# Kernel optimization log

Measured on AMD Instinct MI355X. Metric: run time of the kernel, lower is better.

Reference implementation:

```python
import jax, jax.numpy as jnp
import numpy as np

L = 768
Z_DIM = 128
C = 32
EPS = 1e-5


def _layer_norm(x, w, b):
    mu = jnp.mean(x, axis=-1, keepdims=True)
    var = jnp.mean(jnp.square(x - mu), axis=-1, keepdims=True)
    return (x - mu) * jax.lax.rsqrt(var + EPS) * w + b


def setup_inputs() -> dict:
    key = jax.random.key(0)
    ks = jax.random.split(key, 12)
    s_z = 1.0 / np.sqrt(Z_DIM)
    s_c = 1.0 / np.sqrt(C)
    return {
        "z": jax.random.normal(ks[0], (L, L, Z_DIM), dtype=jnp.float32),
        "norm_w": jnp.ones((Z_DIM,), jnp.float32),
        "norm_b": jnp.zeros((Z_DIM,), jnp.float32),
        "onorm_w": jnp.ones((C,), jnp.float32),
        "onorm_b": jnp.zeros((C,), jnp.float32),
        "a_w": jax.random.normal(ks[1], (C, Z_DIM), jnp.float32) * s_z,
        "a_b": jnp.zeros((C,), jnp.float32),
        "ag_w": jax.random.normal(ks[2], (C, Z_DIM), jnp.float32) * s_z,
        "ag_b": jnp.zeros((C,), jnp.float32),
        "g_w": jax.random.normal(ks[3], (Z_DIM, Z_DIM), jnp.float32) * s_z,
        "g_b": jnp.zeros((Z_DIM,), jnp.float32),
        "o_w": jax.random.normal(ks[4], (Z_DIM, C), jnp.float32) * s_c,
        "o_b": jnp.zeros((Z_DIM,), jnp.float32),
    }


def reference(z, norm_w, norm_b, onorm_w, onorm_b, a_w, a_b, ag_w, ag_b, g_w, g_b, o_w, o_b):
    zn = _layer_norm(z, norm_w, norm_b)                       # [L,L,Z]
    a = (zn @ a_w.T + a_b) * jax.nn.sigmoid(zn @ ag_w.T + ag_b)  # [L,L,C]
    # source computes b with the same (a) projections -> b == a
    o = jnp.einsum('ilc,jlc->ijc', a, a)                      # [L,L,C]
    o = _layer_norm(o, onorm_w, onorm_b)
    o = o @ o_w.T + o_b                                        # [L,L,Z]
    o = o * jax.nn.sigmoid(zn @ g_w.T + g_b)
    return o
```

## Files before the change

kernel.cpp:

```cpp
#include <hip/hip_runtime.h>
#include <math.h>


#define LDIM 768
#define LL   (768 * 768)
#define ZD   128
#define CD   32

typedef __bf16 bf16x8 __attribute__((ext_vector_type(8)));
typedef float  f32x4  __attribute__((ext_vector_type(4)));

__device__ __forceinline__ ushort f2bf(float f) {
    __bf16 h = (__bf16)f;
    return __builtin_bit_cast(ushort, h);
}
__device__ __forceinline__ float bf2f(ushort u) {
    return __builtin_bit_cast(float, ((unsigned)u) << 16);
}
__device__ __forceinline__ float sigm(float x) {
    return __builtin_amdgcn_rcpf(1.0f + __expf(-x));
}

__global__ __launch_bounds__(256) void k0_wfrag(
    const float* __restrict__ aw, const float* __restrict__ agw,
    const float* __restrict__ gw, ushort* __restrict__ wfrag)
{
    const int f = blockIdx.x * 256 + threadIdx.x;
    if (f >= 12 * 4 * 64) return;
    const int n4 = f >> 6, lane = f & 63;
    const int n = n4 >> 2, kk = n4 & 3;
    const int fr = lane & 15, hi = lane >> 4;
    const int ch = n * 16 + fr;
    const int k0 = kk * 32 + hi * 8;
    const float* src = (ch < 32) ? (aw + ch * ZD)
                     : (ch < 64) ? (agw + (ch - 32) * ZD)
                                 : (gw + (ch - 64) * ZD);
    union { ushort us[8]; uint4 q; } pk;
    #pragma unroll
    for (int j = 0; j < 8; ++j) pk.us[j] = f2bf(src[k0 + j]);
    *(uint4*)&wfrag[(size_t)f * 8] = pk.q;
}

__global__ __launch_bounds__(256) void k1_ln_proj(
    const float* __restrict__ z, const float* __restrict__ nw, const float* __restrict__ nb,
    const ushort* __restrict__ wfrag,
    const float* __restrict__ ab, const float* __restrict__ agb, const float* __restrict__ gb,
    ushort* __restrict__ a_t, ushort* __restrict__ gate)
{
    __shared__ ushort zn[64][136];
    __shared__ ushort gl[64][136];

    const int tid = threadIdx.x;
    const int lane = tid & 63, wave = tid >> 6;
    const int fr = lane & 15, hi = lane >> 4;

    const int t0 = (wave < 2) ? wave     : 6 + (wave - 2) * 3;
    const int t1 = (wave < 2) ? wave + 2 : t0 + 1;
    const int t2 = (wave < 2) ? wave + 4 : t0 + 2;

    bf16x8 bv0[4], bv1[4], bv2[4];
    {
        const ushort* wl = wfrag + (size_t)lane * 8;
        #pragma unroll
        for (int kk = 0; kk < 4; ++kk) {
            bv0[kk] = *(const bf16x8*)(wl + (size_t)(t0 * 4 + kk) * 512);
            bv1[kk] = *(const bf16x8*)(wl + (size_t)(t1 * 4 + kk) * 512);
            bv2[kk] = *(const bf16x8*)(wl + (size_t)(t2 * 4 + kk) * 512);
        }
    }

    float abv = 0.f, agbv = 0.f, gbv0 = 0.f, gbv1 = 0.f, gbv2;
    if (wave < 2) {
        abv  = ab[wave * 16 + fr];
        agbv = agb[wave * 16 + fr];
        gbv2 = gb[t2 * 16 - 64 + fr];
    } else {
        gbv0 = gb[t0 * 16 - 64 + fr];
        gbv1 = gb[t1 * 16 - 64 + fr];
        gbv2 = gb[t2 * 16 - 64 + fr];
    }

    const size_t blockrow = (size_t)blockIdx.x * 256;
    const int lr = tid >> 2, seg = tid & 3;

    float4 zreg[8];
    {
        const float4* zp = (const float4*)(z + (blockrow + lr) * ZD + seg * 32);
        #pragma unroll
        for (int q = 0; q < 8; ++q) zreg[q] = zp[q];
    }

    for (int c = 0; c < 4; ++c) {
        __syncthreads();

        {
            float v[32];
            #pragma unroll
            for (int q = 0; q < 8; ++q) {
                v[q * 4 + 0] = zreg[q].x; v[q * 4 + 1] = zreg[q].y;
                v[q * 4 + 2] = zreg[q].z; v[q * 4 + 3] = zreg[q].w;
            }
            float s = 0.f, ss = 0.f;
            #pragma unroll
            for (int e = 0; e < 32; ++e) { s += v[e]; ss += v[e] * v[e]; }
            s += __shfl_xor(s, 1); ss += __shfl_xor(ss, 1);
            s += __shfl_xor(s, 2); ss += __shfl_xor(ss, 2);
            const float mu  = s * (1.f / 128.f);
            const float var = ss * (1.f / 128.f) - mu * mu;
            const float rs  = rsqrtf(var + 1e-5f);
            union { ushort u[32]; uint4 q4[4]; } pk;
            #pragma unroll
            for (int e = 0; e < 32; ++e) {
                const int k = seg * 32 + e;
                pk.u[e] = f2bf((v[e] - mu) * rs * nw[k] + nb[k]);
            }
            #pragma unroll
            for (int q = 0; q < 4; ++q)
                *(uint4*)&zn[lr][seg * 32 + q * 8] = pk.q4[q];
        }

        if (c < 3) {
            const float4* zp = (const float4*)(z + (blockrow + (c + 1) * 64 + lr) * ZD + seg * 32);
            #pragma unroll
            for (int q = 0; q < 8; ++q) zreg[q] = zp[q];
        }
        __syncthreads();

        f32x4 acc0[4], acc1[4], acc2[4];
        #pragma unroll
        for (int m = 0; m < 4; ++m) {
            acc0[m] = (f32x4){0.f, 0.f, 0.f, 0.f};
            acc1[m] = (f32x4){0.f, 0.f, 0.f, 0.f};
            acc2[m] = (f32x4){0.f, 0.f, 0.f, 0.f};
        }
        #pragma unroll
        for (int m = 0; m < 4; ++m) {
            bf16x8 afm[4];
            #pragma unroll
            for (int kk = 0; kk < 4; ++kk)
                afm[kk] = *(const bf16x8*)&zn[m * 16 + fr][kk * 32 + hi * 8];
            #pragma unroll
            for (int kk = 0; kk < 4; ++kk) {
                acc0[m] = __builtin_amdgcn_mfma_f32_16x16x32_bf16(afm[kk], bv0[kk], acc0[m], 0, 0, 0);
                acc1[m] = __builtin_amdgcn_mfma_f32_16x16x32_bf16(afm[kk], bv1[kk], acc1[m], 0, 0, 0);
                acc2[m] = __builtin_amdgcn_mfma_f32_16x16x32_bf16(afm[kk], bv2[kk], acc2[m], 0, 0, 0);
            }
        }

        const size_t rb = blockrow + (size_t)c * 64;
        if (wave < 2) {
            const int ch = wave * 16 + fr;
            #pragma unroll
            for (int m = 0; m < 4; ++m) {
                union { ushort u[4]; uint2 d; } pk;
                #pragma unroll
                for (int q = 0; q < 4; ++q)
                    pk.u[q] = f2bf((acc0[m][q] + abv) * sigm(acc1[m][q] + agbv));
                *(uint2*)&a_t[(size_t)ch * LL + rb + m * 16 + hi * 4] = pk.d;
            }
            const int gch = t2 * 16 - 64 + fr;
            #pragma unroll
            for (int m = 0; m < 4; ++m)
                #pragma unroll
                for (int q = 0; q < 4; ++q)
                    gl[m * 16 + hi * 4 + q][gch] = f2bf(sigm(acc2[m][q] + gbv2));
        } else {
            const int g0 = t0 * 16 - 64 + fr;
            const int g1 = t1 * 16 - 64 + fr;
            const int g2 = t2 * 16 - 64 + fr;
            #pragma unroll
            for (int m = 0; m < 4; ++m)
                #pragma unroll
                for (int q = 0; q < 4; ++q) {
                    const int row = m * 16 + hi * 4 + q;
                    gl[row][g0] = f2bf(sigm(acc0[m][q] + gbv0));
                    gl[row][g1] = f2bf(sigm(acc1[m][q] + gbv1));
                    gl[row][g2] = f2bf(sigm(acc2[m][q] + gbv2));
                }
        }
        __syncthreads();

        #pragma unroll
        for (int it = 0; it < 4; ++it) {
            const int idx = it * 256 + tid;
            const int r = idx >> 4, cq = idx & 15;
            *(uint4*)&gate[(rb + r) * ZD + cq * 8] = *(const uint4*)&gl[r][cq * 8];
        }
    }
}

__global__ __launch_bounds__(256) void k2_einsum(
    const ushort* __restrict__ a_t, ushort* __restrict__ obuf16)
{
    __shared__ ushort As[2][64][32];
    __shared__ ushort Bs[2][64][32];

    const int tid = threadIdx.x;
    const int c = blockIdx.y;
    int p = blockIdx.x, bi = 0;
    while (p >= 12 - bi) { p -= 12 - bi; ++bi; }
    const int bj = bi + p;
    const int i0 = bi * 64, j0 = bj * 64;
    const ushort* base = a_t + (size_t)c * LL;

    const int srow = tid >> 2, scol = (tid & 3) * 8;
    const ushort* gA = base + (size_t)(i0 + srow) * LDIM + scol;
    const ushort* gB = base + (size_t)(j0 + srow) * LDIM + scol;

    const int wave = tid >> 6, lane = tid & 63;
    const int wi = (wave >> 1) * 32, wj = (wave & 1) * 32;
    const int fr = lane & 15, k8 = (lane >> 4) * 8;

    f32x4 acc[2][2];
    #pragma unroll
    for (int m = 0; m < 2; ++m)
        #pragma unroll
        for (int n = 0; n < 2; ++n)
            acc[m][n] = (f32x4){0.f, 0.f, 0.f, 0.f};

    auto stage = [&](int b, int kc) {
        __builtin_amdgcn_global_load_lds(
            (const uint*)(gA + kc * 32), (uint*)&As[b][srow][scol], 16, 0, 0);
        __builtin_amdgcn_global_load_lds(
            (const uint*)(gB + kc * 32), (uint*)&Bs[b][srow][scol], 16, 0, 0);
    };

    stage(0, 0);
    __syncthreads();
    for (int kc = 0; kc < 24; ++kc) {
        const int cur = kc & 1;
        if (kc + 1 < 24) stage(cur ^ 1, kc + 1);

        bf16x8 av[2], bv[2];
        #pragma unroll
        for (int m = 0; m < 2; ++m)
            av[m] = *(const bf16x8*)&As[cur][wi + m * 16 + fr][k8];
        #pragma unroll
        for (int n = 0; n < 2; ++n)
            bv[n] = *(const bf16x8*)&Bs[cur][wj + n * 16 + fr][k8];

        #pragma unroll
        for (int m = 0; m < 2; ++m)
            #pragma unroll
            for (int n = 0; n < 2; ++n)
                acc[m][n] = __builtin_amdgcn_mfma_f32_16x16x32_bf16(
                    av[m], bv[n], acc[m][n], 0, 0, 0);
        __syncthreads();
    }

    ushort* ob = obuf16 + (size_t)c * LL;
    #pragma unroll
    for (int m = 0; m < 2; ++m)
        #pragma unroll
        for (int n = 0; n < 2; ++n) {
            #pragma unroll
            for (int q = 0; q < 4; ++q) {
                const int row = i0 + wi + m * 16 + (lane >> 4) * 4 + q;
                const int col = j0 + wj + n * 16 + fr;
                ob[(size_t)row * LDIM + col] = f2bf(acc[m][n][q]);
            }
            if (bi != bj) {
                const int mrow = j0 + wj + n * 16 + fr;
                const int mcol = i0 + wi + m * 16 + (lane >> 4) * 4;
                union { ushort u[4]; uint2 d; } pk;
                #pragma unroll
                for (int q = 0; q < 4; ++q) pk.u[q] = f2bf(acc[m][n][q]);
                *(uint2*)&ob[(size_t)mrow * LDIM + mcol] = pk.d;
            }
        }
}

__global__ __launch_bounds__(256) void k3_out(
    const ushort* __restrict__ obuf16,
    const float* __restrict__ onw, const float* __restrict__ onb,
    const float* __restrict__ ow,  const float* __restrict__ obias,
    const ushort* __restrict__ gate, float* __restrict__ out)
{
    __shared__ union { float Ol[64][40]; float Res[64][132]; } u;
    __shared__ ushort An[64][36];
    __shared__ ushort Bw[128][36];

    const int tid = threadIdx.x;
    const int lane = tid & 63, wave = tid >> 6;
    const size_t rowbase = (size_t)blockIdx.x * 64;

    #pragma unroll
    for (int cc = 0; cc < 4; ++cc) {
        const int ch = wave * 8 + cc * 2 + (lane >> 5);
        const int r2 = (lane & 31) * 2;
        const uint uu = *(const uint*)&obuf16[(size_t)ch * LL + rowbase + r2];
        u.Ol[r2][ch]     = bf2f((ushort)(uu & 0xffff));
        u.Ol[r2 + 1][ch] = bf2f((ushort)(uu >> 16));
    }
    {
        const int r = tid >> 1, h = tid & 1;
        const float* src = ow + r * CD + h * 16;
        union { ushort us[16]; uint4 q[2]; } pk;
        #pragma unroll
        for (int e = 0; e < 16; ++e) pk.us[e] = f2bf(src[e]);
        *(uint4*)&Bw[r][h * 16]     = pk.q[0];
        *(uint4*)&Bw[r][h * 16 + 8] = pk.q[1];
    }
    __syncthreads();

    {
        const int r = tid >> 2, seg = tid & 3;
        float v[8];
        #pragma unroll
        for (int e = 0; e < 8; ++e) v[e] = u.Ol[r][seg * 8 + e];
        float s = 0.f, ss = 0.f;
        #pragma unroll
        for (int e = 0; e < 8; ++e) { s += v[e]; ss += v[e] * v[e]; }
        s += __shfl_xor(s, 1); ss += __shfl_xor(ss, 1);
        s += __shfl_xor(s, 2); ss += __shfl_xor(ss, 2);
        const float mu  = s * (1.f / 32.f);
        const float var = ss * (1.f / 32.f) - mu * mu;
        const float rs  = rsqrtf(var + 1e-5f);
        union { ushort us[8]; uint4 q; } pk;
        #pragma unroll
        for (int e = 0; e < 8; ++e) {
            const int c = seg * 8 + e;
            pk.us[e] = f2bf((v[e] - mu) * rs * onw[c] + onb[c]);
        }
        *(uint4*)&An[r][seg * 8] = pk.q;
    }
    __syncthreads();

    const int fr = lane & 15, hi = lane >> 4;
    const int wrow = wave * 16;

    const bf16x8 af = *(const bf16x8*)&An[wrow + fr][hi * 8];
    f32x4 acc[8];
    #pragma unroll
    for (int n = 0; n < 8; ++n) {
        const bf16x8 bv = *(const bf16x8*)&Bw[n * 16 + fr][hi * 8];
        acc[n] = __builtin_amdgcn_mfma_f32_16x16x32_bf16(
            af, bv, (f32x4){0.f, 0.f, 0.f, 0.f}, 0, 0, 0);
    }

    #pragma unroll
    for (int n = 0; n < 8; ++n) {
        const int ch = n * 16 + fr;
        const float obv = obias[ch];
        #pragma unroll
        for (int q = 0; q < 4; ++q)
            u.Res[wrow + hi * 4 + q][ch] = acc[n][q] + obv;
    }
    __syncthreads();

    #pragma unroll
    for (int it = 0; it < 8; ++it) {
        const int idx = it * 256 + tid;
        const int r = idx >> 5, cq = (idx & 31) * 4;
        float4 v4 = *(const float4*)&u.Res[r][cq];
        union { uint2 d; ushort us[4]; } g;
        g.d = *(const uint2*)&gate[(rowbase + r) * ZD + cq];
        v4.x *= bf2f(g.us[0]); v4.y *= bf2f(g.us[1]);
        v4.z *= bf2f(g.us[2]); v4.w *= bf2f(g.us[3]);
        *(float4*)&out[(rowbase + r) * ZD + cq] = v4;
    }
}

extern "C" void kernel_launch(void* const* d_in, const int* in_sizes, int n_in,
                              void* d_out, int out_size, void* d_ws, size_t ws_size,
                              hipStream_t stream) {
    (void)in_sizes; (void)n_in; (void)out_size; (void)ws_size;
    const float* z   = (const float*)d_in[0];
    const float* nw  = (const float*)d_in[1];
    const float* nb  = (const float*)d_in[2];
    const float* onw = (const float*)d_in[3];
    const float* onb = (const float*)d_in[4];
    const float* aw  = (const float*)d_in[5];
    const float* ab  = (const float*)d_in[6];
    const float* agw = (const float*)d_in[7];
    const float* agb = (const float*)d_in[8];
    const float* gw  = (const float*)d_in[9];
    const float* gb  = (const float*)d_in[10];
    const float* ow  = (const float*)d_in[11];
    const float* ob  = (const float*)d_in[12];

    char* ws = (char*)d_ws;
    ushort* a_t    = (ushort*)ws;
    ushort* gate   = (ushort*)(ws + 37748736);
    ushort* obuf16 = (ushort*)(ws + 188743680);
    ushort* wfrag  = (ushort*)(ws + 226492416);

    k0_wfrag<<<12, 256, 0, stream>>>(aw, agw, gw, wfrag);
    k1_ln_proj<<<LL / 256, 256, 0, stream>>>(z, nw, nb, wfrag, ab, agb, gb,
                                             a_t, gate);
    k2_einsum<<<dim3(78, 32), 256, 0, stream>>>(a_t, obuf16);
    k3_out<<<LL / 64, 256, 0, stream>>>(obuf16, onw, onb, ow, ob, gate,
                                        (float*)d_out);
}
```

Measured before the change: 280.0 us.

## Precompute output-projection weight fragments and write k3 results directly from MFMA registers

The o_w bf16 conversion moves into the weight-prep kernel so each k3 block loads ready-made MFMA fragments into registers instead of converting and staging the weights in LDS. The MFMA operands are swapped so each lane holds four consecutive output channels of one row. That lets the bias add, gate multiply and float4 store happen straight from the accumulators, dropping the LDS result staging and one barrier. This shrinks LDS use, which may raise occupancy, but the stores per wave are now strided across rows and may coalesce less well.

```diff
diff --git a/kernel.cpp b/kernel.cpp
--- a/kernel.cpp
+++ b/kernel.cpp
@@ -23,22 +23,33 @@
 
 __global__ __launch_bounds__(256) void k0_wfrag(
     const float* __restrict__ aw, const float* __restrict__ agw,
-    const float* __restrict__ gw, ushort* __restrict__ wfrag)
+    const float* __restrict__ gw, const float* __restrict__ ow,
+    ushort* __restrict__ wfrag, ushort* __restrict__ ofrag)
 {
-    const int f = blockIdx.x * 256 + threadIdx.x;
-    if (f >= 12 * 4 * 64) return;
-    const int n4 = f >> 6, lane = f & 63;
-    const int n = n4 >> 2, kk = n4 & 3;
-    const int fr = lane & 15, hi = lane >> 4;
-    const int ch = n * 16 + fr;
-    const int k0 = kk * 32 + hi * 8;
-    const float* src = (ch < 32) ? (aw + ch * ZD)
-                     : (ch < 64) ? (agw + (ch - 32) * ZD)
-                                 : (gw + (ch - 64) * ZD);
+    const int idx = blockIdx.x * 256 + threadIdx.x;
+    if (idx >= 3584) return;
     union { ushort us[8]; uint4 q; } pk;
-    #pragma unroll
-    for (int j = 0; j < 8; ++j) pk.us[j] = f2bf(src[k0 + j]);
-    *(uint4*)&wfrag[(size_t)f * 8] = pk.q;
+    if (idx < 3072) {
+        const int f = idx, n4 = f >> 6, lane = f & 63;
+        const int n = n4 >> 2, kk = n4 & 3;
+        const int fr = lane & 15, hi = lane >> 4;
+        const int ch = n * 16 + fr;
+        const int k0 = kk * 32 + hi * 8;
+        const float* src = (ch < 32) ? (aw + ch * ZD)
+                         : (ch < 64) ? (agw + (ch - 32) * ZD)
+                                     : (gw + (ch - 64) * ZD);
+        #pragma unroll
+        for (int j = 0; j < 8; ++j) pk.us[j] = f2bf(src[k0 + j]);
+        *(uint4*)&wfrag[(size_t)f * 8] = pk.q;
+    } else {
+        const int e = idx - 3072;
+        const int n = e >> 6, lane = e & 63;
+        const int fr = lane & 15, hi = lane >> 4;
+        const float* src = ow + (n * 16 + fr) * CD + hi * 8;
+        #pragma unroll
+        for (int j = 0; j < 8; ++j) pk.us[j] = f2bf(src[j]);
+        *(uint4*)&ofrag[(size_t)e * 8] = pk.q;
+    }
 }
 
 __global__ __launch_bounds__(256) void k1_ln_proj(
@@ -273,33 +284,29 @@
 __global__ __launch_bounds__(256) void k3_out(
     const ushort* __restrict__ obuf16,
     const float* __restrict__ onw, const float* __restrict__ onb,
-    const float* __restrict__ ow,  const float* __restrict__ obias,
+    const ushort* __restrict__ ofrag, const float* __restrict__ obias,
     const ushort* __restrict__ gate, float* __restrict__ out)
 {
-    __shared__ union { float Ol[64][40]; float Res[64][132]; } u;
+    __shared__ float  Ol[64][40];
     __shared__ ushort An[64][36];
-    __shared__ ushort Bw[128][36];
 
     const int tid = threadIdx.x;
     const int lane = tid & 63, wave = tid >> 6;
+    const int fr = lane & 15, hi = lane >> 4;
     const size_t rowbase = (size_t)blockIdx.x * 64;
+
+    bf16x8 ofr[8];
+    #pragma unroll
+    for (int n = 0; n < 8; ++n)
+        ofr[n] = *(const bf16x8*)&ofrag[(size_t)n * 512 + lane * 8];
 
     #pragma unroll
     for (int cc = 0; cc < 4; ++cc) {
         const int ch = wave * 8 + cc * 2 + (lane >> 5);
         const int r2 = (lane & 31) * 2;
         const uint uu = *(const uint*)&obuf16[(size_t)ch * LL + rowbase + r2];
-        u.Ol[r2][ch]     = bf2f((ushort)(uu & 0xffff));
-        u.Ol[r2 + 1][ch] = bf2f((ushort)(uu >> 16));
-    }
-    {
-        const int r = tid >> 1, h = tid & 1;
-        const float* src = ow + r * CD + h * 16;
-        union { ushort us[16]; uint4 q[2]; } pk;
-        #pragma unroll
-        for (int e = 0; e < 16; ++e) pk.us[e] = f2bf(src[e]);
-        *(uint4*)&Bw[r][h * 16]     = pk.q[0];
-        *(uint4*)&Bw[r][h * 16 + 8] = pk.q[1];
+        Ol[r2][ch]     = bf2f((ushort)(uu & 0xffff));
+        Ol[r2 + 1][ch] = bf2f((ushort)(uu >> 16));
     }
     __syncthreads();
 
@@ -307,7 +314,7 @@
         const int r = tid >> 2, seg = tid & 3;
         float v[8];
         #pragma unroll
-        for (int e = 0; e < 8; ++e) v[e] = u.Ol[r][seg * 8 + e];
+        for (int e = 0; e < 8; ++e) v[e] = Ol[r][seg * 8 + e];
         float s = 0.f, ss = 0.f;
         #pragma unroll
         for (int e = 0; e < 8; ++e) { s += v[e]; ss += v[e] * v[e]; }
@@ -326,38 +333,24 @@
     }
     __syncthreads();
 
-    const int fr = lane & 15, hi = lane >> 4;
     const int wrow = wave * 16;
-
     const bf16x8 af = *(const bf16x8*)&An[wrow + fr][hi * 8];
-    f32x4 acc[8];
+    const size_t orow = rowbase + wrow + fr;
+
     #pragma unroll
     for (int n = 0; n < 8; ++n) {
-        const bf16x8 bv = *(const bf16x8*)&Bw[n * 16 + fr][hi * 8];
-        acc[n] = __builtin_amdgcn_mfma_f32_16x16x32_bf16(
-            af, bv, (f32x4){0.f, 0.f, 0.f, 0.f}, 0, 0, 0);
-    }
-
-    #pragma unroll
-    for (int n = 0; n < 8; ++n) {
-        const int ch = n * 16 + fr;
-        const float obv = obias[ch];
-        #pragma unroll
-        for (int q = 0; q < 4; ++q)
-            u.Res[wrow + hi * 4 + q][ch] = acc[n][q] + obv;
-    }
-    __syncthreads();
-
-    #pragma unroll
-    for (int it = 0; it < 8; ++it) {
-        const int idx = it * 256 + tid;
-        const int r = idx >> 5, cq = (idx & 31) * 4;
-        float4 v4 = *(const float4*)&u.Res[r][cq];
+        const f32x4 acc = __builtin_amdgcn_mfma_f32_16x16x32_bf16(
+            ofr[n], af, (f32x4){0.f, 0.f, 0.f, 0.f}, 0, 0, 0);
+        const int ch0 = n * 16 + hi * 4;
+        const float4 ob4 = *(const float4*)&obias[ch0];
         union { uint2 d; ushort us[4]; } g;
-        g.d = *(const uint2*)&gate[(rowbase + r) * ZD + cq];
-        v4.x *= bf2f(g.us[0]); v4.y *= bf2f(g.us[1]);
-        v4.z *= bf2f(g.us[2]); v4.w *= bf2f(g.us[3]);
-        *(float4*)&out[(rowbase + r) * ZD + cq] = v4;
+        g.d = *(const uint2*)&gate[orow * ZD + ch0];
+        float4 w;
+        w.x = (acc[0] + ob4.x) * bf2f(g.us[0]);
+        w.y = (acc[1] + ob4.y) * bf2f(g.us[1]);
+        w.z = (acc[2] + ob4.z) * bf2f(g.us[2]);
+        w.w = (acc[3] + ob4.w) * bf2f(g.us[3]);
+        *(float4*)&out[orow * ZD + ch0] = w;
     }
 }
 
@@ -384,11 +377,12 @@
     ushort* gate   = (ushort*)(ws + 37748736);
     ushort* obuf16 = (ushort*)(ws + 188743680);
     ushort* wfrag  = (ushort*)(ws + 226492416);
-
-    k0_wfrag<<<12, 256, 0, stream>>>(aw, agw, gw, wfrag);
+    ushort* ofrag  = (ushort*)(ws + 226541568);
+
+    k0_wfrag<<<14, 256, 0, stream>>>(aw, agw, gw, ow, wfrag, ofrag);
     k1_ln_proj<<<LL / 256, 256, 0, stream>>>(z, nw, nb, wfrag, ab, agb, gb,
                                              a_t, gate);
     k2_einsum<<<dim3(78, 32), 256, 0, stream>>>(a_t, obuf16);
-    k3_out<<<LL / 64, 256, 0, stream>>>(obuf16, onw, onb, ow, ob, gate,
+    k3_out<<<LL / 64, 256, 0, stream>>>(obuf16, onw, onb, ofrag, ob, gate,
                                         (float*)d_out);
 }
```

New measurement: 299.3 us. +6.9%, slower.
